# Optimization experiments

Measured on AMD Instinct MI355X. Metric: run time of the kernel, lower is better.

The kernel has to match this reference:

```python
import jax, jax.numpy as jnp
import numpy as np

D_MODEL = 768
NUM_HEADS = 12
D_K = D_MODEL // NUM_HEADS


def setup_inputs() -> dict:
    key = jax.random.key(0)
    ks = jax.random.split(key, 8)
    B, S = 2, 2048
    scale = 1.0 / np.sqrt(D_MODEL)
    return {
        "query": jax.random.normal(ks[0], (B, S, D_MODEL), dtype=jnp.float32),
        "key": jax.random.normal(ks[1], (B, S, D_MODEL), dtype=jnp.float32),
        "value": jax.random.normal(ks[2], (B, S, D_MODEL), dtype=jnp.float32),
        "W_q": jax.random.normal(ks[3], (D_MODEL, D_MODEL), dtype=jnp.float32) * scale,
        "W_k": jax.random.normal(ks[4], (D_MODEL, D_MODEL), dtype=jnp.float32) * scale,
        "W_v": jax.random.normal(ks[5], (D_MODEL, D_MODEL), dtype=jnp.float32) * scale,
        "W_o": jax.random.normal(ks[6], (D_MODEL, D_MODEL), dtype=jnp.float32) * scale,
        "b_o": jax.random.normal(ks[7], (D_MODEL,), dtype=jnp.float32) * 0.01,
    }


def reference(query, key, value, W_q, W_k, W_v, W_o, b_o):
    B, S, _ = query.shape
    # Linear weights stored as [in, out] equivalent of torch x @ W.T with W:[out,in]
    def split_heads(x, W):
        # [B,S,D] @ [D,D] -> [B,S,H,dk] -> [B,H,S,dk]
        return (x @ W).reshape(B, S, NUM_HEADS, D_K).transpose(0, 2, 1, 3)

    Q = split_heads(query, W_q)
    K = split_heads(key, W_k)
    V = split_heads(value, W_v)

    scores = jnp.einsum("bhqd,bhkd->bhqk", Q, K) / np.sqrt(D_K)
    attention_weights = jax.nn.softmax(scores, axis=-1)  # [B,H,S,S]
    attn_out = jnp.einsum("bhqk,bhkd->bhqd", attention_weights, V)
    attn_out = attn_out.transpose(0, 2, 1, 3).reshape(B, S, D_MODEL)
    output = attn_out @ W_o + b_o
    return (output, attention_weights)
```

## Files before the change

kernel.cpp:

```cpp
#include <hip/hip_runtime.h>
#include <math.h>

#define D_MODEL 768
#define NUM_HEADS 12
#define D_K 64
#define B_SZ 2
#define S_LEN 2048
#define M_TOT (B_SZ * S_LEN)
#define OUT0 (M_TOT * D_MODEL)
#define BH (B_SZ * NUM_HEADS)
#define WSZ ((size_t)D_MODEL * D_MODEL)
#define PSZ ((size_t)M_TOT * D_MODEL)

#define SWZ(row, off) ((row) * 128 + ((off) ^ (((row) & 7) << 4)))

typedef __attribute__((ext_vector_type(8))) short s16x8;
typedef __attribute__((ext_vector_type(4))) short s16x4;
typedef __attribute__((ext_vector_type(4))) float f32x4;
typedef __attribute__((ext_vector_type(2))) unsigned u32x2;

__device__ __forceinline__ short f2bf(float f) {
    union { float f; unsigned u; } x; x.f = f;
    unsigned r = x.u + 0x7fffu + ((x.u >> 16) & 1u);
    return (short)(r >> 16);
}

__device__ __forceinline__ void gload16(const void* g, void* l) {
    __builtin_amdgcn_global_load_lds(
        (const __attribute__((address_space(1))) unsigned int*)g,
        (__attribute__((address_space(3))) unsigned int*)l, 16, 0, 0);
}

__global__ void cvt_all(const float* __restrict__ q, const float* __restrict__ k,
                        const float* __restrict__ v, short* __restrict__ Xb,
                        const float* __restrict__ W0, const float* __restrict__ W1,
                        const float* __restrict__ W2, const float* __restrict__ W3,
                        short* __restrict__ Wt) {
    const int bx = blockIdx.x;
    const int t = threadIdx.x;
    if (bx < 4608) {
        const int z = bx / 1536, blk = bx - z * 1536;
        const float* src = z == 0 ? q : z == 1 ? k : v;
        const size_t base = ((size_t)blk * 256 + t) * 8;
        float4 v0 = *(const float4*)(src + base);
        float4 v1 = *(const float4*)(src + base + 4);
        s16x8 o;
        o[0] = f2bf(v0.x); o[1] = f2bf(v0.y); o[2] = f2bf(v0.z); o[3] = f2bf(v0.w);
        o[4] = f2bf(v1.x); o[5] = f2bf(v1.y); o[6] = f2bf(v1.z); o[7] = f2bf(v1.w);
        *(s16x8*)(Xb + (size_t)z * PSZ + base) = o;
    } else {
        __shared__ short Ts[64][65];
        const int u = bx - 4608;
        const int z = u / 144, vv = u - z * 144;
        const float* W = z == 0 ? W0 : z == 1 ? W1 : z == 2 ? W2 : W3;
        const float sc = (z == 0) ? 0.125f : 1.0f;
        short* dst = Wt + (size_t)z * WSZ;
        const int k0 = (vv / 12) * 64, n0 = (vv % 12) * 64;
#pragma unroll
        for (int e = 0; e < 16; ++e) {
            int uu = t + 256 * e; int r = uu >> 6, c = uu & 63;
            Ts[c][r] = f2bf(sc * W[(size_t)(k0 + r) * D_MODEL + n0 + c]);
        }
        __syncthreads();
#pragma unroll
        for (int e = 0; e < 16; ++e) {
            int uu = t + 256 * e; int r = uu >> 6, c = uu & 63;
            dst[(size_t)(n0 + r) * D_MODEL + k0 + c] = Ts[r][c];
        }
    }
}

__global__ void proj128(const short* __restrict__ Xb, const short* __restrict__ Wt,
                        short* __restrict__ Yv, short* __restrict__ Vt) {
    __shared__ __align__(16) char As[16384];
    __shared__ __align__(16) char Bs[16384];
    const int t = threadIdx.x, lane = t & 63, w = t >> 6;
    const int l15 = lane & 15, lg = lane >> 4;
    const int wr = w >> 1, wc = w & 1;
    const int m0 = blockIdx.x * 128, n0 = blockIdx.y * 128;
    const int z = blockIdx.z;
    const short* X = Xb + (size_t)z * PSZ;
    const short* W = Wt + (size_t)z * WSZ;

    f32x4 acc[4][4] = {};
    for (int k0 = 0; k0 < D_MODEL; k0 += 64) {
        __syncthreads();
#pragma unroll
        for (int e = 0; e < 4; ++e) {
            int u = t + 256 * e, row = u >> 3, c8 = u & 7;
            s16x8 va = *(const s16x8*)(X + (size_t)(m0 + row) * D_MODEL + k0 + c8 * 8);
            *(s16x8*)(As + SWZ(row, c8 * 16)) = va;
            s16x8 vb = *(const s16x8*)(W + (size_t)(n0 + row) * D_MODEL + k0 + c8 * 8);
            *(s16x8*)(Bs + SWZ(row, c8 * 16)) = vb;
        }
        __syncthreads();
#pragma unroll
        for (int kk = 0; kk < 2; ++kk) {
            const int kb = kk * 64 + lg * 16;
            s16x8 a[4], b[4];
#pragma unroll
            for (int i = 0; i < 4; ++i) {
                int ra = wr * 64 + i * 16 + l15;
                a[i] = *(const s16x8*)(As + SWZ(ra, kb));
                int rb = wc * 64 + i * 16 + l15;
                b[i] = *(const s16x8*)(Bs + SWZ(rb, kb));
            }
#pragma unroll
            for (int i = 0; i < 4; ++i)
#pragma unroll
                for (int j = 0; j < 4; ++j)
                    acc[i][j] = __builtin_amdgcn_mfma_f32_16x16x32_bf16(a[i], b[j], acc[i][j], 0, 0, 0);
        }
    }

    if (z < 2) {
#pragma unroll
        for (int i = 0; i < 4; ++i)
#pragma unroll
            for (int j = 0; j < 4; ++j)
#pragma unroll
                for (int r = 0; r < 4; ++r) {
                    int m = m0 + wr * 64 + i * 16 + lg * 4 + r;
                    int n = n0 + wc * 64 + j * 16 + l15;
                    int b_ = m >> 11, s = m & (S_LEN - 1);
                    int h = n >> 6, dk = n & 63;
                    Yv[(size_t)z * PSZ +
                       (((size_t)(b_ * NUM_HEADS + h) * S_LEN + s) * D_K + dk)] = f2bf(acc[i][j][r]);
                }
    } else {
#pragma unroll
        for (int i = 0; i < 4; ++i)
#pragma unroll
            for (int j = 0; j < 4; ++j) {
                int m = m0 + wr * 64 + i * 16 + lg * 4;
                int n = n0 + wc * 64 + j * 16 + l15;
                int b_ = m >> 11, s = m & (S_LEN - 1);
                int h = n >> 6, dk = n & 63;
                s16x4 pack;
#pragma unroll
                for (int r = 0; r < 4; ++r) pack[r] = f2bf(acc[i][j][r]);
                *(s16x4*)(Vt + ((size_t)(b_ * NUM_HEADS + h) * D_K + dk) * S_LEN + s) = pack;
            }
    }
}

__global__ void proj64o(const short* __restrict__ AO, const short* __restrict__ Wt,
                        const float* __restrict__ bias, float* __restrict__ out) {
    __shared__ __align__(16) char As[8192];
    __shared__ __align__(16) char Bs[8192];
    const int t = threadIdx.x, lane = t & 63, w = t >> 6;
    const int l15 = lane & 15, lg = lane >> 4;
    const int wr = w >> 1, wc = w & 1;
    const int m0 = blockIdx.x * 64, n0 = blockIdx.y * 64;

    const int r8 = t >> 3, c8 = (t & 7) * 8;
    f32x4 acc[2][2] = {};
    for (int k0 = 0; k0 < D_MODEL; k0 += 64) {
        __syncthreads();
        {
            gload16(AO + (size_t)(m0 + r8) * D_MODEL + k0 + c8, As + t * 16);
            gload16(AO + (size_t)(m0 + 32 + r8) * D_MODEL + k0 + c8, As + (t + 256) * 16);
            gload16(Wt + (size_t)(n0 + r8) * D_MODEL + k0 + c8, Bs + t * 16);
            gload16(Wt + (size_t)(n0 + 32 + r8) * D_MODEL + k0 + c8, Bs + (t + 256) * 16);
        }
        __syncthreads();
#pragma unroll
        for (int kk = 0; kk < 2; ++kk) {
            const int kb = kk * 64 + lg * 16;
            s16x8 a[2], b[2];
#pragma unroll
            for (int i = 0; i < 2; ++i) {
                a[i] = *(const s16x8*)(As + (wr * 32 + i * 16 + l15) * 128 + kb);
                b[i] = *(const s16x8*)(Bs + (wc * 32 + i * 16 + l15) * 128 + kb);
            }
#pragma unroll
            for (int i = 0; i < 2; ++i)
#pragma unroll
                for (int j = 0; j < 2; ++j)
                    acc[i][j] = __builtin_amdgcn_mfma_f32_16x16x32_bf16(a[i], b[j], acc[i][j], 0, 0, 0);
        }
    }
#pragma unroll
    for (int i = 0; i < 2; ++i)
#pragma unroll
        for (int j = 0; j < 2; ++j)
#pragma unroll
            for (int r = 0; r < 4; ++r) {
                int m = m0 + wr * 32 + i * 16 + lg * 4 + r;
                int n = n0 + wc * 32 + j * 16 + l15;
                out[(size_t)m * D_MODEL + n] = acc[i][j][r] + bias[n];
            }
}

#define KS(c) (SMEM + (c) * 8192)
#define VS(c) (SMEM + 16384 + (c) * 8192)
#define PS    (SMEM + 32768)
#define KB(c) (SMEM + (c) * 16384)

__global__ __launch_bounds__(256, 4) void attn_fused(const short* __restrict__ Qp,
                                                     const short* __restrict__ Kp,
                                                     const short* __restrict__ Vt,
                                                     float* __restrict__ attn,
                                                     short* __restrict__ AO) {
    __shared__ __align__(16) char SMEM[40960];

    const int t = threadIdx.x, lane = t & 63, w = t >> 6;
    const int l15 = lane & 15, lg = lane >> 4;
    int wg = blockIdx.x;
    wg = (wg & 7) * 96 + (wg >> 3);
    const int q0 = (wg & 31) * 64;
    const int bh = wg >> 5;
    const int b_ = bh / NUM_HEADS, h = bh % NUM_HEADS;
    const short* Qg = Qp + (size_t)bh * S_LEN * D_K;
    const short* Kg = Kp + (size_t)bh * S_LEN * D_K;
    const short* Vg = Vt + (size_t)bh * D_K * S_LEN;
    float* attng = attn + (size_t)bh * S_LEN * S_LEN;
    char* Pw = PS + w * 2048;

    const int r0 = t >> 3, c0 = t & 7;
    const int r1 = (t + 256) >> 3, c1 = t & 7;

    const int qrow = w * 16 + l15;
    const s16x8 qa = *(const s16x8*)(Qg + (size_t)(q0 + qrow) * D_K + lg * 8);
    const s16x8 qb = *(const s16x8*)(Qg + (size_t)(q0 + qrow) * D_K + 32 + lg * 8);

#pragma unroll
    for (int e = 0; e < 4; ++e) {
        int row = r0 + 32 * e;
        s16x8 kv = *(const s16x8*)(Kg + (size_t)row * D_K + c0 * 8);
        *(s16x8*)(KB(0) + SWZ(row, c0 * 16)) = kv;
    }
    __syncthreads();

    float z = 0.f;
    for (int kt2 = 0; kt2 < 16; ++kt2) {
        const int c = kt2 & 1;
        s16x8 nk[4];
        if (kt2 < 15) {
#pragma unroll
            for (int e = 0; e < 4; ++e)
                nk[e] = *(const s16x8*)(Kg + (size_t)((kt2 + 1) * 128 + r0 + 32 * e) * D_K + c0 * 8);
        }
#pragma unroll
        for (int sub = 0; sub < 2; ++sub)
#pragma unroll
            for (int mf = 0; mf < 4; ++mf) {
                int krow = sub * 64 + mf * 16 + l15;
                s16x8 ka = *(const s16x8*)(KB(c) + SWZ(krow, lg * 16));
                s16x8 kb = *(const s16x8*)(KB(c) + SWZ(krow, 64 + lg * 16));
                f32x4 s4 = {};
                s4 = __builtin_amdgcn_mfma_f32_16x16x32_bf16(ka, qa, s4, 0, 0, 0);
                s4 = __builtin_amdgcn_mfma_f32_16x16x32_bf16(kb, qb, s4, 0, 0, 0);
#pragma unroll
                for (int r = 0; r < 4; ++r) z += __expf(s4[r]);
            }
        if (kt2 < 15) {
#pragma unroll
            for (int e = 0; e < 4; ++e)
                *(s16x8*)(KB(c ^ 1) + SWZ(r0 + 32 * e, c0 * 16)) = nk[e];
        }
        __syncthreads();
    }
    z += __shfl_xor(z, 16);
    z += __shfl_xor(z, 32);
    const float invZ = 1.f / z;

    {
        s16x8 k0 = *(const s16x8*)(Kg + (size_t)r0 * D_K + c0 * 8);
        s16x8 k1 = *(const s16x8*)(Kg + (size_t)r1 * D_K + c1 * 8);
        s16x8 v0 = *(const s16x8*)(Vg + (size_t)r0 * S_LEN + c0 * 8);
        s16x8 v1 = *(const s16x8*)(Vg + (size_t)r1 * S_LEN + c1 * 8);
        *(s16x8*)(KS(0) + SWZ(r0, c0 * 16)) = k0;
        *(s16x8*)(KS(0) + SWZ(r1, c1 * 16)) = k1;
        *(s16x8*)(VS(0) + SWZ(r0, c0 * 16)) = v0;
        *(s16x8*)(VS(0) + SWZ(r1, c1 * 16)) = v1;
    }
    __syncthreads();

    f32x4 accO[4] = {};
    for (int kt = 0; kt < 32; ++kt) {
        const int c = kt & 1;
        s16x8 nk0, nk1, nv0, nv1;
        if (kt < 31) {
            nk0 = *(const s16x8*)(Kg + (size_t)((kt + 1) * 64 + r0) * D_K + c0 * 8);
            nk1 = *(const s16x8*)(Kg + (size_t)((kt + 1) * 64 + r1) * D_K + c1 * 8);
            nv0 = *(const s16x8*)(Vg + (size_t)r0 * S_LEN + (kt + 1) * 64 + c0 * 8);
            nv1 = *(const s16x8*)(Vg + (size_t)r1 * S_LEN + (kt + 1) * 64 + c1 * 8);
        }
#pragma unroll
        for (int mf = 0; mf < 4; ++mf) {
            int krow = mf * 16 + l15;
            s16x8 ka = *(const s16x8*)(KS(c) + SWZ(krow, lg * 16));
            s16x8 kb = *(const s16x8*)(KS(c) + SWZ(krow, 64 + lg * 16));
            f32x4 s4 = {};
            s4 = __builtin_amdgcn_mfma_f32_16x16x32_bf16(ka, qa, s4, 0, 0, 0);
            s4 = __builtin_amdgcn_mfma_f32_16x16x32_bf16(kb, qb, s4, 0, 0, 0);
            float p0 = __expf(s4[0]) * invZ;
            float p1 = __expf(s4[1]) * invZ;
            float p2 = __expf(s4[2]) * invZ;
            float p3 = __expf(s4[3]) * invZ;
            unsigned pk0, pk1;
            asm("v_cvt_pk_bf16_f32 %0, %1, %2" : "=v"(pk0) : "v"(p0), "v"(p1));
            asm("v_cvt_pk_bf16_f32 %0, %1, %2" : "=v"(pk1) : "v"(p2), "v"(p3));
            u32x2 pw2 = {pk0, pk1};
            *(u32x2*)(Pw + SWZ(l15, mf * 32 + lg * 8)) = pw2;
        }
        asm volatile("s_waitcnt lgkmcnt(0)" ::: "memory");
        __builtin_amdgcn_sched_barrier(0);
#pragma unroll
        for (int i = 0; i < 4; ++i) {
            int row = i * 4 + lg;
            u32x2 pk = *(const u32x2*)(Pw + SWZ(row, l15 * 8));
            union { unsigned u; float f; } t0, t1, t2, t3;
            t0.u = pk[0] << 16;
            t1.u = pk[0] & 0xFFFF0000u;
            t2.u = pk[1] << 16;
            t3.u = pk[1] & 0xFFFF0000u;
            f32x4 pv = {t0.f, t1.f, t2.f, t3.f};
            *(f32x4*)(attng + (size_t)(q0 + w * 16 + row) * S_LEN + kt * 64 + l15 * 4) = pv;
        }
#pragma unroll
        for (int ks = 0; ks < 2; ++ks) {
            s16x8 ap = *(const s16x8*)(Pw + SWZ(l15, ks * 64 + lg * 16));
#pragma unroll
            for (int df = 0; df < 4; ++df) {
                int vrow = df * 16 + l15;
                s16x8 bv = *(const s16x8*)(VS(c) + SWZ(vrow, ks * 64 + lg * 16));
                accO[df] = __builtin_amdgcn_mfma_f32_16x16x32_bf16(ap, bv, accO[df], 0, 0, 0);
            }
        }
        if (kt < 31) {
            *(s16x8*)(KS(c ^ 1) + SWZ(r0, c0 * 16)) = nk0;
            *(s16x8*)(KS(c ^ 1) + SWZ(r1, c1 * 16)) = nk1;
            *(s16x8*)(VS(c ^ 1) + SWZ(r0, c0 * 16)) = nv0;
            *(s16x8*)(VS(c ^ 1) + SWZ(r1, c1 * 16)) = nv1;
        }
        __syncthreads();
    }

#pragma unroll
    for (int df = 0; df < 4; ++df)
#pragma unroll
        for (int r = 0; r < 4; ++r) {
            int srow = q0 + w * 16 + lg * 4 + r;
            AO[((size_t)(b_ * S_LEN + srow)) * D_MODEL + h * D_K + df * 16 + l15] = f2bf(accO[df][r]);
        }
}

extern "C" void kernel_launch(void* const* d_in, const int* in_sizes, int n_in,
                              void* d_out, int out_size, void* d_ws, size_t ws_size,
                              hipStream_t stream) {
    const float* q = (const float*)d_in[0];
    const float* k = (const float*)d_in[1];
    const float* v = (const float*)d_in[2];
    const float* Wq = (const float*)d_in[3];
    const float* Wk = (const float*)d_in[4];
    const float* Wv = (const float*)d_in[5];
    const float* Wo = (const float*)d_in[6];
    const float* bo = (const float*)d_in[7];

    float* out = (float*)d_out;
    float* attn = (float*)d_out + OUT0;

    short* Xb = (short*)attn;

    short* wsS = (short*)d_ws;
    short* Wtq = wsS;
    short* Qp = Wtq + 4 * WSZ;
    short* Kp = Qp + PSZ;
    short* Vtg = Kp + PSZ;
    short* AO = Vtg + PSZ;

    dim3 blk(256);

    cvt_all<<<dim3(5184), blk, 0, stream>>>(q, k, v, Xb, Wq, Wk, Wv, Wo, Wtq);

    proj128<<<dim3(M_TOT / 128, D_MODEL / 128, 3), blk, 0, stream>>>(Xb, Wtq, Qp, Vtg);

    attn_fused<<<dim3(768), blk, 0, stream>>>(Qp, Kp, Vtg, attn, AO);

    proj64o<<<dim3(M_TOT / 64, D_MODEL / 64), blk, 0, stream>>>(AO, Wtq + 3 * WSZ, bo, out);
}
```

Measured before the change: 169.8 us.

## Fold log2e into Q scale, use exp2 with log-normalizer bias, nontemporal stores

Pre-scales W_q by log2(e)/8 so scores are already in base-2 units, which lets the kernel use raw v_exp_f32 instead of __expf. The normalization by 1/Z becomes a -log2(Z) accumulator initializer in the MFMA, so no multiply is needed per element. The row-sum is spread over four partial accumulators to shorten the dependency chain. The large attention-weight and output writes use nontemporal stores to reduce cache pollution. These changes rely on scores staying bounded without max subtraction, the same assumption the code already made.

Measured after the change: 151.0 us. -11.1%, faster.

```diff
diff --git a/kernel.cpp b/kernel.cpp
--- a/kernel.cpp
+++ b/kernel.cpp
@@ -23,6 +23,14 @@
     union { float f; unsigned u; } x; x.f = f;
     unsigned r = x.u + 0x7fffu + ((x.u >> 16) & 1u);
     return (short)(r >> 16);
+}
+
+__device__ __forceinline__ float fexp2(float x) {
+#if __has_builtin(__builtin_amdgcn_exp2f)
+    return __builtin_amdgcn_exp2f(x);
+#else
+    float r; asm("v_exp_f32 %0, %1" : "=v"(r) : "v"(x)); return r;
+#endif
 }
 
 __device__ __forceinline__ void gload16(const void* g, void* l) {
@@ -53,7 +61,7 @@
         const int u = bx - 4608;
         const int z = u / 144, vv = u - z * 144;
         const float* W = z == 0 ? W0 : z == 1 ? W1 : z == 2 ? W2 : W3;
-        const float sc = (z == 0) ? 0.125f : 1.0f;
+        const float sc = (z == 0) ? 0.18033688011112042f : 1.0f;
         short* dst = Wt + (size_t)z * WSZ;
         const int k0 = (vv / 12) * 64, n0 = (vv % 12) * 64;
 #pragma unroll
@@ -188,7 +196,8 @@
             for (int r = 0; r < 4; ++r) {
                 int m = m0 + wr * 32 + i * 16 + lg * 4 + r;
                 int n = n0 + wc * 32 + j * 16 + l15;
-                out[(size_t)m * D_MODEL + n] = acc[i][j][r] + bias[n];
+                __builtin_nontemporal_store(acc[i][j][r] + bias[n],
+                                            out + (size_t)m * D_MODEL + n);
             }
 }
 
@@ -232,7 +241,7 @@
     }
     __syncthreads();
 
-    float z = 0.f;
+    f32x4 zv = {};
     for (int kt2 = 0; kt2 < 16; ++kt2) {
         const int c = kt2 & 1;
         s16x8 nk[4];
@@ -252,7 +261,7 @@
                 s4 = __builtin_amdgcn_mfma_f32_16x16x32_bf16(ka, qa, s4, 0, 0, 0);
                 s4 = __builtin_amdgcn_mfma_f32_16x16x32_bf16(kb, qb, s4, 0, 0, 0);
 #pragma unroll
-                for (int r = 0; r < 4; ++r) z += __expf(s4[r]);
+                for (int r = 0; r < 4; ++r) zv[r] += fexp2(s4[r]);
             }
         if (kt2 < 15) {
 #pragma unroll
@@ -261,9 +270,10 @@
         }
         __syncthreads();
     }
+    float z = (zv[0] + zv[1]) + (zv[2] + zv[3]);
     z += __shfl_xor(z, 16);
     z += __shfl_xor(z, 32);
-    const float invZ = 1.f / z;
+    const float mlz = -__log2f(z);
 
     {
         s16x8 k0 = *(const s16x8*)(Kg + (size_t)r0 * D_K + c0 * 8);
@@ -292,13 +302,13 @@
             int krow = mf * 16 + l15;
             s16x8 ka = *(const s16x8*)(KS(c) + SWZ(krow, lg * 16));
             s16x8 kb = *(const s16x8*)(KS(c) + SWZ(krow, 64 + lg * 16));
-            f32x4 s4 = {};
+            f32x4 s4 = {mlz, mlz, mlz, mlz};
             s4 = __builtin_amdgcn_mfma_f32_16x16x32_bf16(ka, qa, s4, 0, 0, 0);
             s4 = __builtin_amdgcn_mfma_f32_16x16x32_bf16(kb, qb, s4, 0, 0, 0);
-            float p0 = __expf(s4[0]) * invZ;
-            float p1 = __expf(s4[1]) * invZ;
-            float p2 = __expf(s4[2]) * invZ;
-            float p3 = __expf(s4[3]) * invZ;
+            float p0 = fexp2(s4[0]);
+            float p1 = fexp2(s4[1]);
+            float p2 = fexp2(s4[2]);
+            float p3 = fexp2(s4[3]);
             unsigned pk0, pk1;
             asm("v_cvt_pk_bf16_f32 %0, %1, %2" : "=v"(pk0) : "v"(p0), "v"(p1));
             asm("v_cvt_pk_bf16_f32 %0, %1, %2" : "=v"(pk1) : "v"(p2), "v"(p3));
@@ -317,7 +327,8 @@
             t2.u = pk[1] << 16;
             t3.u = pk[1] & 0xFFFF0000u;
             f32x4 pv = {t0.f, t1.f, t2.f, t3.f};
-            *(f32x4*)(attng + (size_t)(q0 + w * 16 + row) * S_LEN + kt * 64 + l15 * 4) = pv;
+            __builtin_nontemporal_store(
+                pv, (f32x4*)(attng + (size_t)(q0 + w * 16 + row) * S_LEN + kt * 64 + l15 * 4));
         }
 #pragma unroll
         for (int ks = 0; ks < 2; ++ks) {
```
